# Kernel optimization log

Measured on AMD Instinct MI355X. Metric: run time of the kernel, lower is better.

The kernel has to match this reference:

```python
import jax, jax.numpy as jnp
import numpy as np

IMG_SIZE = 500
FM = 31
RATIOS = [1.0, 2.0, 0.5]
SCALES = [128, 256, 512]
PRE_NMS_TOPN = 6000
POST_NMS_TOPN = 1500
IOU_THRESHOLD = 0.7
VARIANCES = (0.1, 0.1, 0.2, 0.2)
BATCH = 64
TOTAL_ANCHORS = FM * FM * len(RATIOS) * len(SCALES)  # 8649


def generate_anchors():
    # normalized [y1, x1, y2, x2] anchors on a FM x FM grid
    stride = 1.0 / FM
    ctr = (np.arange(FM, dtype=np.float32) + 0.5) * stride
    cx, cy = np.meshgrid(ctr, ctr)
    centers = np.stack([cy.ravel(), cx.ravel()], axis=-1)  # [FM*FM, 2] (cy, cx)
    hs, ws = [], []
    for scale in SCALES:
        for ratio in RATIOS:
            ws.append((scale * np.sqrt(ratio)) / IMG_SIZE)
            hs.append((scale / np.sqrt(ratio)) / IMG_SIZE)
    hw = np.stack([np.array(hs, np.float32), np.array(ws, np.float32)], axis=-1)  # [9, 2]
    mins = centers[:, None, :] - hw[None] / 2.0
    maxs = centers[:, None, :] + hw[None] / 2.0
    boxes = np.concatenate([mins, maxs], axis=-1).reshape(-1, 4)  # [A, 4]
    return np.clip(boxes, 0.0, 1.0).astype(np.float32)


def delta_to_bbox(anchors, deltas):
    # anchors: [A,4], deltas: [B,A,4] (dy, dx, dh, dw) -> [B,A,4] (y1,x1,y2,x2)
    anc_h = anchors[:, 2] - anchors[:, 0]
    anc_w = anchors[:, 3] - anchors[:, 1]
    anc_cy = anchors[:, 0] + 0.5 * anc_h
    anc_cx = anchors[:, 1] + 0.5 * anc_w
    h = jnp.exp(deltas[..., 2]) * anc_h
    w = jnp.exp(deltas[..., 3]) * anc_w
    cy = deltas[..., 0] * anc_h + anc_cy
    cx = deltas[..., 1] * anc_w + anc_cx
    return jnp.stack([cy - 0.5 * h, cx - 0.5 * w, cy + 0.5 * h, cx + 0.5 * w], axis=-1)


def pairwise_iou_one_vs_all(sel_box, boxes):
    # sel_box: [B,1,4], boxes: [B,N,4] -> iou [B,N]
    y1 = jnp.maximum(sel_box[..., 0], boxes[..., 0])
    x1 = jnp.maximum(sel_box[..., 1], boxes[..., 1])
    y2 = jnp.minimum(sel_box[..., 2], boxes[..., 2])
    x2 = jnp.minimum(sel_box[..., 3], boxes[..., 3])
    inter = jnp.maximum(y2 - y1, 0.0) * jnp.maximum(x2 - x1, 0.0)
    area_s = (sel_box[..., 2] - sel_box[..., 0]) * (sel_box[..., 3] - sel_box[..., 1])
    area_b = (boxes[..., 2] - boxes[..., 0]) * (boxes[..., 3] - boxes[..., 1])
    return inter / (area_s + area_b - inter + 1e-9)


def batched_greedy_nms(boxes, scores, max_out, iou_threshold):
    # boxes [B,N,4], scores [B,N]; greedy NMS, vectorized over batch, scan over picks
    B, N, _ = boxes.shape

    def step(active, _):
        masked = jnp.where(active, scores, -jnp.inf)            # [B,N]
        idx = jnp.argmax(masked, axis=1)                         # [B]
        sel_score = jnp.take_along_axis(masked, idx[:, None], axis=1)[:, 0]
        sel_box = jnp.take_along_axis(boxes, idx[:, None, None], axis=1)  # [B,1,4]
        iou = pairwise_iou_one_vs_all(sel_box, boxes)            # [B,N]
        active = active & (iou <= iou_threshold)
        valid = jnp.isfinite(sel_score)
        out_box = jnp.where(valid[:, None], sel_box[:, 0, :], 0.0)
        out_score = jnp.where(valid, sel_score, 0.0)
        return active, (out_box, out_score)

    active0 = jnp.ones((B, N), dtype=bool)
    _, (out_boxes, out_scores) = jax.lax.scan(step, active0, None, length=max_out)
    out_boxes = jnp.transpose(out_boxes, (1, 0, 2))   # [B,max_out,4]
    out_scores = jnp.transpose(out_scores, (1, 0))    # [B,max_out]
    # tf.image.combined_non_max_suppression clips output boxes to [0,1] by default
    return jnp.clip(out_boxes, 0.0, 1.0), out_scores


def setup_inputs() -> dict:
    key = jax.random.key(0)
    k1, k2, k3 = jax.random.split(key, 3)
    rpn_bbox_deltas = jax.random.normal(k1, (BATCH, FM, FM, 36), dtype=jnp.float32)
    rpn_probs = jax.random.uniform(k2, (BATCH, FM, FM, 9), dtype=jnp.float32)
    gt_labels = jax.random.randint(k3, (BATCH, 10), 0, 20).astype(jnp.int64)
    anchors = jnp.asarray(generate_anchors())
    return {"rpn_bbox_deltas": rpn_bbox_deltas, "rpn_probs": rpn_probs,
            "gt_labels": gt_labels, "anchors": anchors}


def reference(rpn_bbox_deltas, rpn_probs, gt_labels, anchors):
    B = rpn_bbox_deltas.shape[0]
    A = anchors.shape[0]
    variances = jnp.asarray(VARIANCES, dtype=rpn_bbox_deltas.dtype)
    deltas = rpn_bbox_deltas.reshape(B, A, 4) * variances
    probs = rpn_probs.reshape(B, A)
    rpn_bboxes = delta_to_bbox(anchors, deltas)              # [B,A,4]
    top_scores, top_idx = jax.lax.top_k(probs, PRE_NMS_TOPN)  # sorted desc
    top_boxes = jnp.take_along_axis(rpn_bboxes, top_idx[:, :, None], axis=1)
    roi_bboxes, roi_scores = batched_greedy_nms(top_boxes, top_scores,
                                                POST_NMS_TOPN, IOU_THRESHOLD)
    return roi_bboxes, roi_scores
```

## Files before the change

kernel.cpp:

```cpp
#include <hip/hip_runtime.h>
#include <math.h>

typedef unsigned int u32;
typedef unsigned short u16;
typedef unsigned long long u64;

#define BATCH 64
#define A_TOT 8649
#define TOPN  6000
#define POST  1500
#define NB    4096
#define NT    512
#define NSLOT 12
#define NOACT 0xFFFFFFFFu

#define LDS_BYTES 156064

__global__ __launch_bounds__(NT, 2) void roibbox_kernel(
    const float* __restrict__ deltas,
    const float* __restrict__ probs,
    const float* __restrict__ anchors,
    float* __restrict__ out)
{
    #pragma clang fp contract(off)
    __shared__ alignas(16) char smem[LDS_BYTES];
    u64*    keysL   = (u64*)   (smem + 0);
    float4* boxes4  = (float4*)(smem + 48000);
    u32*    bucketA = (u32*)   (smem + 69632);
    u32*    bucketB = (u32*)   (smem + 86016);
    u32*    stemp   = (u32*)   (smem + 102400);
    u16*    ppL     = (u16*)   (smem + 144000);
    u32*    wminL   = (u32*)   (smem + 156000);

    const int tid = threadIdx.x;
    const int b   = blockIdx.x;
    const float* pb = probs + (size_t)b * A_TOT;

    #pragma unroll
    for (int i = 0; i < NB/NT; ++i) bucketA[tid + i*NT] = 0u;
    __syncthreads();

    for (int j = tid; j < A_TOT; j += NT) {
        float s = pb[j];
        int bkt = (int)(s * (float)NB);
        bkt = (NB-1) - min(max(bkt, 0), NB-1);
        atomicAdd(&bucketA[bkt], 1u);
    }
    __syncthreads();

    {
        int base8 = tid << 3;
        u32 c[8]; u32 ms = 0;
        #pragma unroll
        for (int i = 0; i < 8; ++i) { c[i] = bucketA[base8+i]; ms += c[i]; }
        stemp[tid] = ms;
        __syncthreads();
        int src = 0;
        for (int off = 1; off < NT; off <<= 1) {
            u32 v = stemp[src*NT + tid];
            if (tid >= off) v += stemp[src*NT + tid - off];
            stemp[(src^1)*NT + tid] = v;
            __syncthreads();
            src ^= 1;
        }
        u32 excl = stemp[src*NT + tid] - ms;
        #pragma unroll
        for (int i = 0; i < 8; ++i) {
            bucketA[base8+i] = excl; bucketB[base8+i] = excl; excl += c[i];
        }
    }
    __syncthreads();

    for (int j = tid; j < A_TOT; j += NT) {
        float s = pb[j];
        int bkt = (int)(s * (float)NB);
        bkt = (NB-1) - min(max(bkt, 0), NB-1);
        u32 pos = atomicAdd(&bucketB[bkt], 1u);
        keysL[pos] = ((u64)__float_as_uint(s) << 32) | (u64)(~(u32)j);
    }
    __syncthreads();

    for (int bkt = tid; bkt < NB; bkt += NT) {
        int begin = (int)bucketA[bkt], end = (int)bucketB[bkt];
        for (int k = begin + 1; k < end; ++k) {
            u64 key = keysL[k];
            int m = k - 1;
            while (m >= begin && keysL[m] < key) { keysL[m+1] = keysL[m]; --m; }
            keysL[m+1] = key;
        }
    }
    __syncthreads();

    float ry1[NSLOT], rx1[NSLOT], ry2[NSLOT], rx2[NSLOT], rA[NSLOT];
    u32 mask = 0;
    const u32 base = (u32)tid * NSLOT;
    if (tid < TOPN / NSLOT) {
        #pragma unroll
        for (int i = 0; i < NSLOT; ++i) {
            int j = (int)base + i;
            u64 k = keysL[j];
            u32 aidx = ~((u32)k);
            float4 av = *(const float4*)(anchors + (size_t)aidx * 4);
            float4 dv = *(const float4*)(deltas + ((size_t)b * A_TOT + aidx) * 4);
            float d0 = dv.x*0.1f, d1 = dv.y*0.1f, d2 = dv.z*0.2f, d3 = dv.w*0.2f;
            float ah = av.z - av.x, aw = av.w - av.y;
            float acy = av.x + 0.5f*ah, acx = av.y + 0.5f*aw;
            float h = (float)exp((double)d2) * ah;
            float w = (float)exp((double)d3) * aw;
            float cy = d0*ah + acy;
            float cx = d1*aw + acx;
            ry1[i] = cy - 0.5f*h; rx1[i] = cx - 0.5f*w;
            ry2[i] = cy + 0.5f*h; rx2[i] = cx + 0.5f*w;
            rA[i]  = (ry2[i]-ry1[i])*(rx2[i]-rx1[i]);
            boxes4[j] = make_float4(ry1[i], rx1[i], ry2[i], rx2[i]);
        }
        mask = (1u << NSLOT) - 1u;
    } else {
        #pragma unroll
        for (int i = 0; i < NSLOT; ++i) { ry1[i]=0.f; rx1[i]=0.f; ry2[i]=0.f; rx2[i]=0.f; rA[i]=0.f; }
    }
    for (int j = tid; j < TOPN/2; j += NT) ((u32*)ppL)[j] = 0xFFFFFFFFu;
    __syncthreads();

    const double MTHR = (double)0.7f + 0x1p-25;
    const u32 lane = (u32)tid & 63u;
    const u32 wv   = (u32)tid >> 6;
    u32 cur = 0;
    int pend = POST;

    for (int p = 0; p < POST; ++p) {
        u32* wslot = wminL + (p & 1) * 8;
        u64 anyb = __ballot(mask != 0u);
        if (anyb != 0ull) {
            if (cur - base < (u32)NSLOT) ppL[cur] = (u16)p;
            float4 sb = boxes4[cur];
            float sA = (sb.z - sb.x) * (sb.w - sb.y);
            #pragma unroll
            for (int i = 0; i < NSLOT; ++i) {
                float yy1 = fmaxf(sb.x, ry1[i]);
                float xx1 = fmaxf(sb.y, rx1[i]);
                float yy2 = fminf(sb.z, ry2[i]);
                float xx2 = fminf(sb.w, rx2[i]);
                float inter = fmaxf(yy2 - yy1, 0.0f) * fmaxf(xx2 - xx1, 0.0f);
                float den = ((sA + rA[i]) - inter) + 1e-9f;
                if ((double)inter >= MTHR * (double)den) mask &= ~(1u << i);
            }
            u64 bal = __ballot(mask != 0u);
            if (mask != 0u) {
                if (lane == (u32)__builtin_ctzll(bal))
                    wslot[wv] = base + (u32)__builtin_ctz(mask);
            } else if (bal == 0ull) {
                if (lane == 0u) wslot[wv] = NOACT;
            }
        } else {
            if (lane == 0u) wslot[wv] = NOACT;
        }
        __syncthreads();
        uint4 wa = *((const uint4*)wslot);
        uint4 wb = *((const uint4*)(wslot + 4));
        u32 g = min(min(min(wa.x, wa.y), min(wa.z, wa.w)),
                    min(min(wb.x, wb.y), min(wb.z, wb.w)));
        if (g == NOACT) { pend = p + 1; break; }
        cur = g;
    }

    const size_t sbase = (size_t)BATCH * POST * 4;
    if (tid < TOPN / NSLOT) {
        #pragma unroll
        for (int i = 0; i < NSLOT; ++i) {
            u32 v = (u32)ppL[base + i];
            if (v != 0xFFFFu) {
                size_t row = (size_t)b * POST + v;
                float* ob = out + row * 4;
                ob[0] = fminf(fmaxf(ry1[i], 0.f), 1.f);
                ob[1] = fminf(fmaxf(rx1[i], 0.f), 1.f);
                ob[2] = fminf(fmaxf(ry2[i], 0.f), 1.f);
                ob[3] = fminf(fmaxf(rx2[i], 0.f), 1.f);
                out[sbase + row] = __uint_as_float((u32)(keysL[base + i] >> 32));
            }
        }
    }
    for (int r = pend + tid; r < POST; r += NT) {
        size_t row = (size_t)b * POST + r;
        float* ob = out + row * 4;
        ob[0]=0.f; ob[1]=0.f; ob[2]=0.f; ob[3]=0.f;
        out[sbase + row] = 0.f;
    }
}

extern "C" void kernel_launch(void* const* d_in, const int* in_sizes, int n_in,
                              void* d_out, int out_size, void* d_ws, size_t ws_size,
                              hipStream_t stream) {
    const float* deltas  = (const float*)d_in[0];
    const float* probs   = (const float*)d_in[1];
    const float* anchors = (const float*)d_in[3];
    float* out = (float*)d_out;

    roibbox_kernel<<<dim3(BATCH), dim3(NT), 0, stream>>>(deltas, probs, anchors, out);
}
```

Before: 1.494 ms.

## Replace per-pick block barriers in NMS with wave-pipelined frontier ring buffer

Greedy NMS previously ran a __syncthreads and an LDS min-reduction for every selected box. Now a single frontier wave owns the lowest-ranked live candidates, picks winners and pushes them into an LDS ring with release atomics. The other waves consume that ring asynchronously and take over as frontier once all lower waves are exhausted. The candidate layout changes to wave-contiguous, lane-strided ranks so each wave covers a contiguous rank range, and slot-level ballots let fully dead slots be skipped. This removes block-wide barriers from the serial loop at the cost of spin-polling, s_sleep, priority tweaks and more complex memory-ordering logic.

```diff
diff --git a/kernel.cpp b/kernel.cpp
--- a/kernel.cpp
+++ b/kernel.cpp
@@ -11,10 +11,13 @@
 #define POST  1500
 #define NB    4096
 #define NT    512
+#define NWAVE 8
 #define NSLOT 12
-#define NOACT 0xFFFFFFFFu
-
-#define LDS_BYTES 156064
+#define DONEBIT 0x80000000u
+#define CNTMASK 0x7FFFFFFFu
+#define GUARD_MAX (1 << 17)
+
+#define LDS_BYTES 106496
 
 __global__ __launch_bounds__(NT, 2) void roibbox_kernel(
     const float* __restrict__ deltas,
@@ -25,15 +28,18 @@
     #pragma clang fp contract(off)
     __shared__ alignas(16) char smem[LDS_BYTES];
     u64*    keysL   = (u64*)   (smem + 0);
-    float4* boxes4  = (float4*)(smem + 48000);
     u32*    bucketA = (u32*)   (smem + 69632);
     u32*    bucketB = (u32*)   (smem + 86016);
     u32*    stemp   = (u32*)   (smem + 102400);
-    u16*    ppL     = (u16*)   (smem + 144000);
-    u32*    wminL   = (u32*)   (smem + 156000);
+    float4* ringL   = (float4*)(smem + 69632);
+    u16*    ppL     = (u16*)   (smem + 93632);
+    u32*    ctrlP   = (u32*)   (smem + 105632);
+    u32*    ctrlF   = (u32*)   (smem + 105636);
 
     const int tid = threadIdx.x;
     const int b   = blockIdx.x;
+    const u32 lane = (u32)tid & 63u;
+    const u32 w    = (u32)tid >> 6;
     const float* pb = probs + (size_t)b * A_TOT;
 
     #pragma unroll
@@ -93,12 +99,12 @@
 
     float ry1[NSLOT], rx1[NSLOT], ry2[NSLOT], rx2[NSLOT], rA[NSLOT];
     u32 mask = 0;
-    const u32 base = (u32)tid * NSLOT;
-    if (tid < TOPN / NSLOT) {
-        #pragma unroll
-        for (int i = 0; i < NSLOT; ++i) {
-            int j = (int)base + i;
-            u64 k = keysL[j];
+    #pragma unroll
+    for (int i = 0; i < NSLOT; ++i) {
+        u32 r = w*768u + (u32)i*64u + lane;
+        ry1[i]=0.f; rx1[i]=0.f; ry2[i]=0.f; rx2[i]=0.f; rA[i]=0.f;
+        if (r < TOPN) {
+            u64 k = keysL[r];
             u32 aidx = ~((u32)k);
             float4 av = *(const float4*)(anchors + (size_t)aidx * 4);
             float4 dv = *(const float4*)(deltas + ((size_t)b * A_TOT + aidx) * 4);
@@ -106,69 +112,149 @@
             float ah = av.z - av.x, aw = av.w - av.y;
             float acy = av.x + 0.5f*ah, acx = av.y + 0.5f*aw;
             float h = (float)exp((double)d2) * ah;
-            float w = (float)exp((double)d3) * aw;
+            float wd = (float)exp((double)d3) * aw;
             float cy = d0*ah + acy;
             float cx = d1*aw + acx;
-            ry1[i] = cy - 0.5f*h; rx1[i] = cx - 0.5f*w;
-            ry2[i] = cy + 0.5f*h; rx2[i] = cx + 0.5f*w;
+            ry1[i] = cy - 0.5f*h;  rx1[i] = cx - 0.5f*wd;
+            ry2[i] = cy + 0.5f*h;  rx2[i] = cx + 0.5f*wd;
             rA[i]  = (ry2[i]-ry1[i])*(rx2[i]-rx1[i]);
-            boxes4[j] = make_float4(ry1[i], rx1[i], ry2[i], rx2[i]);
-        }
-        mask = (1u << NSLOT) - 1u;
-    } else {
+            mask |= 1u << i;
+        }
+    }
+    u32 slotAlive = 0;
+    #pragma unroll
+    for (int i = 0; i < NSLOT; ++i)
+        if (__ballot((mask >> i) & 1u)) slotAlive |= 1u << i;
+
+    for (int j = tid; j < TOPN/2; j += NT) ((u32*)ppL)[j] = 0xFFFFFFFFu;
+    if (tid == 0) { *ctrlP = 0u; *ctrlF = 0u; }
+    __syncthreads();
+
+    const double MTHR = (double)0.7f + 0x1p-25;
+
+    auto suppress_all = [&](float sy1, float sx1, float sy2, float sx2, float sA) {
+        u32 na = 0;
         #pragma unroll
-        for (int i = 0; i < NSLOT; ++i) { ry1[i]=0.f; rx1[i]=0.f; ry2[i]=0.f; rx2[i]=0.f; rA[i]=0.f; }
-    }
-    for (int j = tid; j < TOPN/2; j += NT) ((u32*)ppL)[j] = 0xFFFFFFFFu;
-    __syncthreads();
-
-    const double MTHR = (double)0.7f + 0x1p-25;
-    const u32 lane = (u32)tid & 63u;
-    const u32 wv   = (u32)tid >> 6;
-    u32 cur = 0;
-    int pend = POST;
-
-    for (int p = 0; p < POST; ++p) {
-        u32* wslot = wminL + (p & 1) * 8;
-        u64 anyb = __ballot(mask != 0u);
-        if (anyb != 0ull) {
-            if (cur - base < (u32)NSLOT) ppL[cur] = (u16)p;
-            float4 sb = boxes4[cur];
-            float sA = (sb.z - sb.x) * (sb.w - sb.y);
-            #pragma unroll
-            for (int i = 0; i < NSLOT; ++i) {
-                float yy1 = fmaxf(sb.x, ry1[i]);
-                float xx1 = fmaxf(sb.y, rx1[i]);
-                float yy2 = fminf(sb.z, ry2[i]);
-                float xx2 = fminf(sb.w, rx2[i]);
+        for (int i = 0; i < NSLOT; ++i) {
+            if (slotAlive & (1u << i)) {
+                float yy1 = fmaxf(sy1, ry1[i]);
+                float xx1 = fmaxf(sx1, rx1[i]);
+                float yy2 = fminf(sy2, ry2[i]);
+                float xx2 = fminf(sx2, rx2[i]);
                 float inter = fmaxf(yy2 - yy1, 0.0f) * fmaxf(xx2 - xx1, 0.0f);
                 float den = ((sA + rA[i]) - inter) + 1e-9f;
                 if ((double)inter >= MTHR * (double)den) mask &= ~(1u << i);
-            }
-            u64 bal = __ballot(mask != 0u);
-            if (mask != 0u) {
-                if (lane == (u32)__builtin_ctzll(bal))
-                    wslot[wv] = base + (u32)__builtin_ctz(mask);
-            } else if (bal == 0ull) {
-                if (lane == 0u) wslot[wv] = NOACT;
-            }
-        } else {
-            if (lane == 0u) wslot[wv] = NOACT;
-        }
-        __syncthreads();
-        uint4 wa = *((const uint4*)wslot);
-        uint4 wb = *((const uint4*)(wslot + 4));
-        u32 g = min(min(min(wa.x, wa.y), min(wa.z, wa.w)),
-                    min(min(wb.x, wb.y), min(wb.z, wb.w)));
-        if (g == NOACT) { pend = p + 1; break; }
-        cur = g;
-    }
+                if (__ballot((mask >> i) & 1u)) na |= 1u << i;
+            }
+        }
+        slotAlive = na;
+    };
+
+    bool frontier = (w == 0);
+    u32 consumed = 0, pc = 0;
+    const u32 mybit = 1u << w;
+    if (frontier) __builtin_amdgcn_s_setprio(1);
+
+    for (int guard = 0; guard < GUARD_MAX; ++guard) {
+        if (frontier) {
+            if (!slotAlive) {
+                __builtin_amdgcn_s_setprio(0);
+                u32 old = __hip_atomic_fetch_or(ctrlF, mybit, __ATOMIC_ACQ_REL,
+                                                __HIP_MEMORY_SCOPE_WORKGROUP);
+                if ((old | mybit) == (1u << NWAVE) - 1u) {
+                    u32 c = __hip_atomic_load(ctrlP, __ATOMIC_ACQUIRE,
+                                              __HIP_MEMORY_SCOPE_WORKGROUP);
+                    __hip_atomic_store(ctrlP, c | DONEBIT, __ATOMIC_RELEASE,
+                                       __HIP_MEMORY_SCOPE_WORKGROUP);
+                }
+                break;
+            }
+            u32 fs = (u32)__builtin_ctz(slotAlive);
+            u64 fb = __ballot((mask >> fs) & 1u);
+            u32 ol = (u32)__builtin_ctzll(fb);
+            u32 rank = w*768u + fs*64u + ol;
+            float ey, ex, ez, ew2;
+            switch (fs) {
+                case 0:  ey=ry1[0];  ex=rx1[0];  ez=ry2[0];  ew2=rx2[0];  break;
+                case 1:  ey=ry1[1];  ex=rx1[1];  ez=ry2[1];  ew2=rx2[1];  break;
+                case 2:  ey=ry1[2];  ex=rx1[2];  ez=ry2[2];  ew2=rx2[2];  break;
+                case 3:  ey=ry1[3];  ex=rx1[3];  ez=ry2[3];  ew2=rx2[3];  break;
+                case 4:  ey=ry1[4];  ex=rx1[4];  ez=ry2[4];  ew2=rx2[4];  break;
+                case 5:  ey=ry1[5];  ex=rx1[5];  ez=ry2[5];  ew2=rx2[5];  break;
+                case 6:  ey=ry1[6];  ex=rx1[6];  ez=ry2[6];  ew2=rx2[6];  break;
+                case 7:  ey=ry1[7];  ex=rx1[7];  ez=ry2[7];  ew2=rx2[7];  break;
+                case 8:  ey=ry1[8];  ex=rx1[8];  ez=ry2[8];  ew2=rx2[8];  break;
+                case 9:  ey=ry1[9];  ex=rx1[9];  ez=ry2[9];  ew2=rx2[9];  break;
+                case 10: ey=ry1[10]; ex=rx1[10]; ez=ry2[10]; ew2=rx2[10]; break;
+                default: ey=ry1[11]; ex=rx1[11]; ez=ry2[11]; ew2=rx2[11]; break;
+            }
+            if (lane == ol) {
+                ppL[rank] = (u16)pc;
+                ringL[pc] = make_float4(ey, ex, ez, ew2);
+            }
+            float sy1 = __shfl(ey,  (int)ol);
+            float sx1 = __shfl(ex,  (int)ol);
+            float sy2 = __shfl(ez,  (int)ol);
+            float sx2 = __shfl(ew2, (int)ol);
+            u32 np = pc + 1;
+            __hip_atomic_store(ctrlP, np | ((np >= POST) ? DONEBIT : 0u),
+                               __ATOMIC_RELEASE, __HIP_MEMORY_SCOPE_WORKGROUP);
+            float sA = (sy2 - sy1) * (sx2 - sx1);
+            suppress_all(sy1, sx1, sy2, sx2, sA);
+            pc = np; consumed = np;
+            if (np >= POST) break;
+            continue;
+        }
+        u32 pv = __hip_atomic_load(ctrlP, __ATOMIC_ACQUIRE, __HIP_MEMORY_SCOPE_WORKGROUP);
+        u32 cnt = pv & CNTMASK;
+        if (cnt > consumed) {
+            float4 e = ringL[consumed];
+            for (;;) {
+                float4 en = e;
+                if (consumed + 1 < cnt) en = ringL[consumed + 1];
+                float sA = (e.z - e.x) * (e.w - e.y);
+                suppress_all(e.x, e.y, e.z, e.w, sA);
+                ++consumed;
+                if (consumed >= cnt) break;
+                e = en;
+            }
+            if (!slotAlive) {
+                u32 old = __hip_atomic_fetch_or(ctrlF, mybit, __ATOMIC_ACQ_REL,
+                                                __HIP_MEMORY_SCOPE_WORKGROUP);
+                if ((old | mybit) == (1u << NWAVE) - 1u) {
+                    u32 c = __hip_atomic_load(ctrlP, __ATOMIC_ACQUIRE,
+                                              __HIP_MEMORY_SCOPE_WORKGROUP);
+                    __hip_atomic_store(ctrlP, c | DONEBIT, __ATOMIC_RELEASE,
+                                       __HIP_MEMORY_SCOPE_WORKGROUP);
+                }
+                break;
+            }
+            continue;
+        }
+        if (pv & DONEBIT) break;
+        u32 fl = __hip_atomic_load(ctrlF, __ATOMIC_ACQUIRE, __HIP_MEMORY_SCOPE_WORKGROUP);
+        u32 below = mybit - 1u;
+        if ((fl & below) == below) {
+            u32 pv2 = __hip_atomic_load(ctrlP, __ATOMIC_ACQUIRE, __HIP_MEMORY_SCOPE_WORKGROUP);
+            if (pv2 & DONEBIT) break;
+            if ((pv2 & CNTMASK) == consumed) {
+                frontier = true; pc = consumed;
+                __builtin_amdgcn_s_setprio(1);
+            }
+            continue;
+        }
+        __builtin_amdgcn_s_sleep(1);
+    }
+    __builtin_amdgcn_s_setprio(0);
+    __syncthreads();
+    u32 pend = (*ctrlP) & CNTMASK;
 
     const size_t sbase = (size_t)BATCH * POST * 4;
-    if (tid < TOPN / NSLOT) {
-        #pragma unroll
-        for (int i = 0; i < NSLOT; ++i) {
-            u32 v = (u32)ppL[base + i];
+    #pragma unroll
+    for (int i = 0; i < NSLOT; ++i) {
+        u32 r = w*768u + (u32)i*64u + lane;
+        if (r < TOPN) {
+            u32 v = (u32)ppL[r];
             if (v != 0xFFFFu) {
                 size_t row = (size_t)b * POST + v;
                 float* ob = out + row * 4;
@@ -176,12 +262,12 @@
                 ob[1] = fminf(fmaxf(rx1[i], 0.f), 1.f);
                 ob[2] = fminf(fmaxf(ry2[i], 0.f), 1.f);
                 ob[3] = fminf(fmaxf(rx2[i], 0.f), 1.f);
-                out[sbase + row] = __uint_as_float((u32)(keysL[base + i] >> 32));
-            }
-        }
-    }
-    for (int r = pend + tid; r < POST; r += NT) {
-        size_t row = (size_t)b * POST + r;
+                out[sbase + row] = __uint_as_float((u32)(keysL[r] >> 32));
+            }
+        }
+    }
+    for (int p = (int)pend + tid; p < POST; p += NT) {
+        size_t row = (size_t)b * POST + p;
         float* ob = out + row * 4;
         ob[0]=0.f; ob[1]=0.f; ob[2]=0.f; ob[3]=0.f;
         out[sbase + row] = 0.f;
```

Measured after the change: 1.854 ms. 24.1% more time.

## Replace barrier-per-pick greedy NMS with producer/helper wavefront pipeline over chunks

Applied to the files above, without the earlier changes.

The greedy NMS loop used to do one block-wide barrier per selected box, with every thread holding 12 boxes in registers. Now a single leader wavefront walks 64-box chunks in score order, picks survivors with ballots and appends them to an LDS ring. Fifteen helper wavefronts pre-apply the published picks to upcoming chunks and hand over the finished survivor masks through workgroup-scope atomic flags. This removes the per-iteration __syncthreads and cross-wave min reduction, at the cost of spin-waits, a single-CU block of 1024 threads, and tricky memory-ordering correctness.

```diff
diff --git a/kernel.cpp b/kernel.cpp
--- a/kernel.cpp
+++ b/kernel.cpp
@@ -10,13 +10,18 @@
 #define TOPN  6000
 #define POST  1500
 #define NB    4096
-#define NT    512
-#define NSLOT 12
-#define NOACT 0xFFFFFFFFu
-
-#define LDS_BYTES 156064
-
-__global__ __launch_bounds__(NT, 2) void roibbox_kernel(
+#define NT    1024
+#define NHELP 15
+#define NCHUNK 94
+#define DONEBIT 0x80000000u
+#define CNTMASK 0x7FFFFFFFu
+#define FINALBIT 1u
+#define GUARD_MAX (1 << 18)
+#define SECSTEP 128u
+
+#define LDS_BYTES 148224
+
+__global__ __launch_bounds__(NT) void roibbox_kernel(
     const float* __restrict__ deltas,
     const float* __restrict__ probs,
     const float* __restrict__ anchors,
@@ -25,15 +30,22 @@
     #pragma clang fp contract(off)
     __shared__ alignas(16) char smem[LDS_BYTES];
     u64*    keysL   = (u64*)   (smem + 0);
-    float4* boxes4  = (float4*)(smem + 48000);
     u32*    bucketA = (u32*)   (smem + 69632);
     u32*    bucketB = (u32*)   (smem + 86016);
     u32*    stemp   = (u32*)   (smem + 102400);
-    u16*    ppL     = (u16*)   (smem + 144000);
-    u32*    wminL   = (u32*)   (smem + 156000);
+    u32*    scoresU = (u32*)   (smem + 0);
+    float4* boxesL  = (float4*)(smem + 24064);
+    float4* ringL   = (float4*)(smem + 120064);
+    u16*    prankL  = (u16*)   (smem + 144064);
+    u64*    cmaskL  = (u64*)   (smem + 147072);
+    u32*    applL   = (u32*)   (smem + 147824);
+    u32*    ctrlP   = (u32*)   (smem + 148200);
+    u32*    torchL  = (u32*)   (smem + 148204);
 
     const int tid = threadIdx.x;
     const int b   = blockIdx.x;
+    const u32 lane = (u32)tid & 63u;
+    const u32 w    = (u32)tid >> 6;
     const float* pb = probs + (size_t)b * A_TOT;
 
     #pragma unroll
@@ -49,10 +61,10 @@
     __syncthreads();
 
     {
-        int base8 = tid << 3;
-        u32 c[8]; u32 ms = 0;
-        #pragma unroll
-        for (int i = 0; i < 8; ++i) { c[i] = bucketA[base8+i]; ms += c[i]; }
+        int base4 = tid << 2;
+        u32 c0 = bucketA[base4+0], c1 = bucketA[base4+1],
+            c2 = bucketA[base4+2], c3 = bucketA[base4+3];
+        u32 ms = c0 + c1 + c2 + c3;
         stemp[tid] = ms;
         __syncthreads();
         int src = 0;
@@ -64,10 +76,10 @@
             src ^= 1;
         }
         u32 excl = stemp[src*NT + tid] - ms;
-        #pragma unroll
-        for (int i = 0; i < 8; ++i) {
-            bucketA[base8+i] = excl; bucketB[base8+i] = excl; excl += c[i];
-        }
+        bucketA[base4+0] = excl; bucketB[base4+0] = excl; excl += c0;
+        bucketA[base4+1] = excl; bucketB[base4+1] = excl; excl += c1;
+        bucketA[base4+2] = excl; bucketB[base4+2] = excl; excl += c2;
+        bucketA[base4+3] = excl; bucketB[base4+3] = excl;
     }
     __syncthreads();
 
@@ -91,97 +103,226 @@
     }
     __syncthreads();
 
-    float ry1[NSLOT], rx1[NSLOT], ry2[NSLOT], rx2[NSLOT], rA[NSLOT];
-    u32 mask = 0;
-    const u32 base = (u32)tid * NSLOT;
-    if (tid < TOPN / NSLOT) {
-        #pragma unroll
-        for (int i = 0; i < NSLOT; ++i) {
-            int j = (int)base + i;
-            u64 k = keysL[j];
+    u64 kreg[6];
+    #pragma unroll
+    for (int i = 0; i < 6; ++i) {
+        int r = tid + i*NT;
+        kreg[i] = (r < TOPN) ? keysL[r] : 0ull;
+    }
+    __syncthreads();
+    #pragma unroll
+    for (int i = 0; i < 6; ++i) {
+        int r = tid + i*NT;
+        if (r < TOPN) {
+            u64 k = kreg[i];
             u32 aidx = ~((u32)k);
+            scoresU[r] = (u32)(k >> 32);
             float4 av = *(const float4*)(anchors + (size_t)aidx * 4);
             float4 dv = *(const float4*)(deltas + ((size_t)b * A_TOT + aidx) * 4);
             float d0 = dv.x*0.1f, d1 = dv.y*0.1f, d2 = dv.z*0.2f, d3 = dv.w*0.2f;
             float ah = av.z - av.x, aw = av.w - av.y;
             float acy = av.x + 0.5f*ah, acx = av.y + 0.5f*aw;
-            float h = (float)exp((double)d2) * ah;
-            float w = (float)exp((double)d3) * aw;
+            float h  = (float)exp((double)d2) * ah;
+            float wd = (float)exp((double)d3) * aw;
             float cy = d0*ah + acy;
             float cx = d1*aw + acx;
-            ry1[i] = cy - 0.5f*h; rx1[i] = cx - 0.5f*w;
-            ry2[i] = cy + 0.5f*h; rx2[i] = cx + 0.5f*w;
-            rA[i]  = (ry2[i]-ry1[i])*(rx2[i]-rx1[i]);
-            boxes4[j] = make_float4(ry1[i], rx1[i], ry2[i], rx2[i]);
-        }
-        mask = (1u << NSLOT) - 1u;
+            boxesL[r] = make_float4(cy - 0.5f*h, cx - 0.5f*wd,
+                                    cy + 0.5f*h, cx + 0.5f*wd);
+        }
+    }
+    if (tid < NCHUNK) {
+        cmaskL[tid] = (tid == NCHUNK-1) ? ((1ull << 48) - 1ull) : ~0ull;
+        applL[tid] = 0u;
+    }
+    if (tid == 0) { *ctrlP = 0u; *torchL = 0u; }
+    __syncthreads();
+
+    const double MTHR = (double)0.7f + 0x1p-25;
+
+    if (w == 0) {
+        u32 pc = 0;
+        bool done = false;
+        for (u32 s = 0; s < NCHUNK && !done; ++s) {
+            for (int gg = 0; gg < GUARD_MAX; ++gg) {
+                u32 a = __hip_atomic_load(&applL[s], __ATOMIC_ACQUIRE,
+                                          __HIP_MEMORY_SCOPE_WORKGROUP);
+                if (a & FINALBIT) break;
+                if (gg >= 128) __builtin_amdgcn_s_sleep(1);
+            }
+            u64 am = cmaskL[s];
+            if (am) {
+                __builtin_amdgcn_s_setprio(1);
+                u32 r = s*64u + lane;
+                float4 bx = (r < TOPN) ? boxesL[r] : make_float4(0.f,0.f,0.f,0.f);
+                float bA = (bx.z - bx.x) * (bx.w - bx.y);
+                while (am) {
+                    u32 ol = (u32)__builtin_ctzll(am);
+                    float sy1 = __uint_as_float((u32)__builtin_amdgcn_readlane((int)__float_as_uint(bx.x), (int)ol));
+                    float sx1 = __uint_as_float((u32)__builtin_amdgcn_readlane((int)__float_as_uint(bx.y), (int)ol));
+                    float sy2 = __uint_as_float((u32)__builtin_amdgcn_readlane((int)__float_as_uint(bx.z), (int)ol));
+                    float sx2 = __uint_as_float((u32)__builtin_amdgcn_readlane((int)__float_as_uint(bx.w), (int)ol));
+                    if (lane == ol) {
+                        prankL[pc] = (u16)r;
+                        ringL[pc] = bx;
+                    }
+                    float sA = (sy2 - sy1) * (sx2 - sx1);
+                    float yy1 = fmaxf(sy1, bx.x);
+                    float xx1 = fmaxf(sx1, bx.y);
+                    float yy2 = fminf(sy2, bx.z);
+                    float xx2 = fminf(sx2, bx.w);
+                    float inter = fmaxf(yy2 - yy1, 0.f) * fmaxf(xx2 - xx1, 0.f);
+                    float den = ((sA + bA) - inter) + 1e-9f;
+                    u64 supp = __ballot((double)inter >= MTHR * (double)den);
+                    am &= ~supp;
+                    ++pc;
+                    if (pc >= POST) {
+                        if (lane == 0)
+                            __hip_atomic_store(ctrlP, pc | DONEBIT, __ATOMIC_RELEASE,
+                                               __HIP_MEMORY_SCOPE_WORKGROUP);
+                        done = true;
+                        break;
+                    }
+                    if ((pc & 3u) == 0u && lane == 0)
+                        __hip_atomic_store(ctrlP, pc, __ATOMIC_RELEASE,
+                                           __HIP_MEMORY_SCOPE_WORKGROUP);
+                }
+                __builtin_amdgcn_s_setprio(0);
+            }
+            if (!done && lane == 0) {
+                __hip_atomic_store(ctrlP, pc, __ATOMIC_RELEASE,
+                                   __HIP_MEMORY_SCOPE_WORKGROUP);
+                __hip_atomic_store(torchL, s + 1u, __ATOMIC_RELEASE,
+                                   __HIP_MEMORY_SCOPE_WORKGROUP);
+            }
+        }
+        if (!done && lane == 0)
+            __hip_atomic_store(ctrlP, pc | DONEBIT, __ATOMIC_RELEASE,
+                               __HIP_MEMORY_SCOPE_WORKGROUP);
     } else {
-        #pragma unroll
-        for (int i = 0; i < NSLOT; ++i) { ry1[i]=0.f; rx1[i]=0.f; ry2[i]=0.f; rx2[i]=0.f; rA[i]=0.f; }
-    }
-    for (int j = tid; j < TOPN/2; j += NT) ((u32*)ppL)[j] = 0xFFFFFFFFu;
-    __syncthreads();
-
-    const double MTHR = (double)0.7f + 0x1p-25;
-    const u32 lane = (u32)tid & 63u;
-    const u32 wv   = (u32)tid >> 6;
-    u32 cur = 0;
-    int pend = POST;
-
-    for (int p = 0; p < POST; ++p) {
-        u32* wslot = wminL + (p & 1) * 8;
-        u64 anyb = __ballot(mask != 0u);
-        if (anyb != 0ull) {
-            if (cur - base < (u32)NSLOT) ppL[cur] = (u16)p;
-            float4 sb = boxes4[cur];
-            float sA = (sb.z - sb.x) * (sb.w - sb.y);
-            #pragma unroll
-            for (int i = 0; i < NSLOT; ++i) {
-                float yy1 = fmaxf(sb.x, ry1[i]);
-                float xx1 = fmaxf(sb.y, rx1[i]);
-                float yy2 = fminf(sb.z, ry2[i]);
-                float xx2 = fminf(sb.w, rx2[i]);
-                float inter = fmaxf(yy2 - yy1, 0.0f) * fmaxf(xx2 - xx1, 0.0f);
-                float den = ((sA + rA[i]) - inter) + 1e-9f;
-                if ((double)inter >= MTHR * (double)den) mask &= ~(1u << i);
-            }
-            u64 bal = __ballot(mask != 0u);
-            if (mask != 0u) {
-                if (lane == (u32)__builtin_ctzll(bal))
-                    wslot[wv] = base + (u32)__builtin_ctz(mask);
-            } else if (bal == 0ull) {
-                if (lane == 0u) wslot[wv] = NOACT;
-            }
+        u32 h = w - 1;
+        u32 s  = h;
+        u32 sn = h + NHELP;
+        float4 bxA, bxB; float aA = 0.f, aB = 0.f;
+        u32 alA = 0u, alB = 0u, myA = 0u, myB = 0u;
+        {
+            u32 r = s*64u + lane;
+            bxA = (r < TOPN) ? boxesL[r] : make_float4(0.f,0.f,0.f,0.f);
+            aA = (bxA.z - bxA.x) * (bxA.w - bxA.y);
+            alA = (r < TOPN) ? 1u : 0u;
+        }
+        if (sn < NCHUNK) {
+            u32 r = sn*64u + lane;
+            bxB = (r < TOPN) ? boxesL[r] : make_float4(0.f,0.f,0.f,0.f);
+            aB = (bxB.z - bxB.x) * (bxB.w - bxB.y);
+            alB = (r < TOPN) ? 1u : 0u;
         } else {
-            if (lane == 0u) wslot[wv] = NOACT;
-        }
-        __syncthreads();
-        uint4 wa = *((const uint4*)wslot);
-        uint4 wb = *((const uint4*)(wslot + 4));
-        u32 g = min(min(min(wa.x, wa.y), min(wa.z, wa.w)),
-                    min(min(wb.x, wb.y), min(wb.z, wb.w)));
-        if (g == NOACT) { pend = p + 1; break; }
-        cur = g;
-    }
+            bxB = make_float4(0.f,0.f,0.f,0.f);
+        }
+
+        auto apply_range = [&](const float4& B, float BA, u32& AL, u32 from, u32 to) {
+            u32 q = from;
+            if (q >= to) return;
+            float4 e0 = ringL[q];
+            float4 e1 = (q+1 < to) ? ringL[q+1] : e0;
+            for (; q < to; ++q) {
+                float4 e = e0; e0 = e1;
+                if (q+2 < to) e1 = ringL[q+2];
+                float sA = (e.z - e.x) * (e.w - e.y);
+                float yy1 = fmaxf(e.x, B.x);
+                float xx1 = fmaxf(e.y, B.y);
+                float yy2 = fminf(e.z, B.z);
+                float xx2 = fminf(e.w, B.w);
+                float inter = fmaxf(yy2 - yy1, 0.f) * fmaxf(xx2 - xx1, 0.f);
+                float den = ((sA + BA) - inter) + 1e-9f;
+                if ((double)inter >= MTHR * (double)den) AL = 0u;
+            }
+        };
+        auto finalize = [&](u32 cs, u64 am) {
+            if (lane == 0) {
+                cmaskL[cs] = am;
+                __hip_atomic_store(&applL[cs], FINALBIT, __ATOMIC_RELEASE,
+                                   __HIP_MEMORY_SCOPE_WORKGROUP);
+            }
+        };
+        auto promote = [&]() -> bool {
+            if (sn >= NCHUNK) return false;
+            s = sn; bxA = bxB; aA = aB; alA = alB; myA = myB;
+            sn = s + NHELP;
+            if (sn < NCHUNK) {
+                u32 r = sn*64u + lane;
+                bxB = (r < TOPN) ? boxesL[r] : make_float4(0.f,0.f,0.f,0.f);
+                aB = (bxB.z - bxB.x) * (bxB.w - bxB.y);
+                alB = (r < TOPN) ? 1u : 0u;
+            } else {
+                alB = 0u;
+            }
+            myB = 0u;
+            return true;
+        };
+
+        bool active = true;
+        for (int it = 0; it < GUARD_MAX && active; ++it) {
+            u32 t    = __hip_atomic_load(torchL, __ATOMIC_ACQUIRE, __HIP_MEMORY_SCOPE_WORKGROUP);
+            u32 pubv = __hip_atomic_load(ctrlP,  __ATOMIC_ACQUIRE, __HIP_MEMORY_SCOPE_WORKGROUP);
+            u32 pub  = pubv & CNTMASK;
+            bool did = false;
+
+            if (pub > myA) {
+                apply_range(bxA, aA, alA, myA, pub);
+                myA = pub;
+                did = true;
+                if (!__ballot(alA)) {
+                    finalize(s, 0ull);
+                    active = promote();
+                    continue;
+                }
+            }
+            if (pubv & DONEBIT) break;
+            if (t >= s) {
+                finalize(s, __ballot(alA));
+                active = promote();
+                continue;
+            }
+            if (sn < NCHUNK && myB < myA) {
+                u32 tgt = myA; u32 lim = myB + SECSTEP;
+                if (lim < tgt) tgt = lim;
+                apply_range(bxB, aB, alB, myB, tgt);
+                myB = tgt;
+                did = true;
+                if (!__ballot(alB)) {
+                    finalize(sn, 0ull);
+                    sn += NHELP;
+                    if (sn < NCHUNK) {
+                        u32 r = sn*64u + lane;
+                        bxB = (r < TOPN) ? boxesL[r] : make_float4(0.f,0.f,0.f,0.f);
+                        aB = (bxB.z - bxB.x) * (bxB.w - bxB.y);
+                        alB = (r < TOPN) ? 1u : 0u;
+                    } else {
+                        alB = 0u;
+                    }
+                    myB = 0u;
+                }
+            }
+            if (!did) __builtin_amdgcn_s_sleep(1);
+        }
+    }
+    __syncthreads();
+    u32 pend = (*ctrlP) & CNTMASK;
 
     const size_t sbase = (size_t)BATCH * POST * 4;
-    if (tid < TOPN / NSLOT) {
-        #pragma unroll
-        for (int i = 0; i < NSLOT; ++i) {
-            u32 v = (u32)ppL[base + i];
-            if (v != 0xFFFFu) {
-                size_t row = (size_t)b * POST + v;
-                float* ob = out + row * 4;
-                ob[0] = fminf(fmaxf(ry1[i], 0.f), 1.f);
-                ob[1] = fminf(fmaxf(rx1[i], 0.f), 1.f);
-                ob[2] = fminf(fmaxf(ry2[i], 0.f), 1.f);
-                ob[3] = fminf(fmaxf(rx2[i], 0.f), 1.f);
-                out[sbase + row] = __uint_as_float((u32)(keysL[base + i] >> 32));
-            }
-        }
-    }
-    for (int r = pend + tid; r < POST; r += NT) {
-        size_t row = (size_t)b * POST + r;
+    for (u32 p = (u32)tid; p < pend; p += NT) {
+        float4 e = ringL[p];
+        u32 rr = (u32)prankL[p];
+        size_t row = (size_t)b * POST + p;
+        float* ob = out + row * 4;
+        ob[0] = fminf(fmaxf(e.x, 0.f), 1.f);
+        ob[1] = fminf(fmaxf(e.y, 0.f), 1.f);
+        ob[2] = fminf(fmaxf(e.z, 0.f), 1.f);
+        ob[3] = fminf(fmaxf(e.w, 0.f), 1.f);
+        out[sbase + row] = __uint_as_float(scoresU[rr]);
+    }
+    for (u32 p = pend + (u32)tid; p < POST; p += NT) {
+        size_t row = (size_t)b * POST + p;
         float* ob = out + row * 4;
         ob[0]=0.f; ob[1]=0.f; ob[2]=0.f; ob[3]=0.f;
         out[sbase + row] = 0.f;
```

After: 1.532 ms. +2.6%, slower.
